# Kernel optimization log

Hardware: AMD Instinct MI355X
Metric: run time of the kernel (lower is better)

Reference implementation:

```python
import jax, jax.numpy as jnp
import numpy as np

H, W, C = 512, 512, 64
N_BOXES = 512
OUT_W = 32


def setup_inputs() -> dict:
    key = jax.random.key(0)
    k1, k2 = jax.random.split(key)
    feature_map = jax.random.normal(k1, (H, W, C), dtype=jnp.float32)
    # boxes are [cx, cy, w, h] as fractions of the image; uniform(0,1) is valid
    boxes = jax.random.uniform(k2, (N_BOXES, 4), dtype=jnp.float32)
    return {"feature_map": feature_map, "boxes": boxes, "output_width": OUT_W}


def reference(feature_map, boxes, output_width):
    """RoIAlign over a batch of boxes (vectorized version of roi_align_batch_serial)."""
    in_h, in_w, c = feature_map.shape
    out_h = out_w = output_width

    def roi_align_single(box):
        cx, cy, w, h = jnp.split(box, 4, axis=-1)
        x0 = cx - w / 2
        y0 = cy - h / 2
        w = jnp.maximum(w, 1e-6)
        h = jnp.maximum(h, 1e-6)
        x_scale = out_w / (w * in_w)
        y_scale = out_h / (h * in_h)
        return jax.image.scale_and_translate(
            feature_map,
            shape=(out_h, out_w, c),
            spatial_dims=(0, 1),
            scale=jnp.concatenate((y_scale, x_scale)),
            translation=jnp.concatenate((-y0 * out_h / h, -x0 * out_w / w)),
            method="linear",
            precision=jax.lax.Precision("fastest"),
        )

    # Same math as jax.lax.map(roi_align_single, boxes), but batched across boxes.
    return jax.vmap(roi_align_single)(boxes)  # [N, out_h, out_w, C]
```

## Files before the change

### kernel.cpp

```cpp
#include <hip/hip_runtime.h>


#define H_IN 512
#define W_IN 512
#define CH   64
#define NB   512
#define OW   32
#define WSTRIDE 33
#define WXS     40
#define TAPS_MAX 33
#define COLS_H  156
#define COLS_CL 146

__global__ __launch_bounds__(256) void roi_weights(const float* __restrict__ boxes,
                                                   float* __restrict__ wTab,
                                                   int* __restrict__ meta) {
    int tid = blockIdx.x * blockDim.x + threadIdx.x;
    if (tid >= NB * 2 * 32) return;
    int o   = tid & 31;
    int dim = (tid >> 5) & 1;
    int b   = tid >> 6;

    float cx = boxes[b * 4 + 0];
    float cy = boxes[b * 4 + 1];
    float bw = boxes[b * 4 + 2];
    float bh = boxes[b * 4 + 3];
    float cc = dim ? cx : cy;
    float sz = dim ? bw : bh;
    float lo = cc - sz * 0.5f;
    sz = fmaxf(sz, 1e-6f);

    float scale = (float)OW / (sz * (float)W_IN);
    float inv   = 1.0f / scale;
    float trans = (-lo * (float)OW) / sz;
    float s     = ((float)o + 0.5f) * inv - trans * inv - 0.5f;
    float ks    = fmaxf(inv, 1.0f);

    int i_lo = max((int)ceilf(s - ks), 0);
    int i_hi = min((int)floorf(s + ks), W_IN - 1);
    int cnt  = i_hi - i_lo + 1;
    if (cnt < 0) cnt = 0;
    if (cnt > TAPS_MAX) cnt = TAPS_MAX;

    float sum = 0.0f;
    for (int k = 0; k < cnt; ++k) {
        float x = fabsf(s - (float)(i_lo + k)) / ks;
        sum += fmaxf(0.0f, 1.0f - x);
    }
    bool ok = (sum > 1.1920929e-4f) && (s >= -0.5f) && (s <= (float)W_IN - 0.5f);

    float* wout = wTab + ((size_t)(dim * NB + b) * 32 + o) * WSTRIDE;
    for (int k = 0; k < TAPS_MAX; ++k) {
        float w = 0.0f;
        if (ok && k < cnt) {
            float x = fabsf(s - (float)(i_lo + k)) / ks;
            w = fmaxf(0.0f, 1.0f - x) / sum;
        }
        wout[k] = w;
    }
    int* m = meta + ((size_t)(dim * NB + b) * 32 + o) * 2;
    m[0] = i_lo;
    m[1] = ok ? cnt : 0;
}

__device__ __forceinline__ void gload16(const float* src, float* ldsDst) {
    __builtin_amdgcn_global_load_lds((const __attribute__((address_space(1))) void*)src,
                                     (__attribute__((address_space(3))) void*)ldsDst, 16, 0, 0);
}

__global__ __launch_bounds__(64) void roi_wave(const float* __restrict__ fm,
                                               const float* __restrict__ wTab,
                                               const int* __restrict__ meta,
                                               float* __restrict__ out) {
    __shared__ float sBuf[2][COLS_H * 16];
    __shared__ float sWx[8 * WXS];
    __shared__ float sWy[16 * WSTRIDE];
    __shared__ int   sMx[16];
    __shared__ int   sMyLC[16];
    __shared__ int   sU[4];

    int bid = blockIdx.x;
    int box = ((bid >> 8) << 3) | (bid & 7);
    int sub = (bid >> 3) & 31;
    int ox0 = (sub & 3) * 8;
    int ch0 = ((sub >> 2) & 3) * 16;
    int oy0 = (sub >> 4) * 16;
    int t   = threadIdx.x;

    const float* wxsrc = wTab + ((size_t)(NB + box) * 32 + ox0) * WSTRIDE;
    for (int i = t; i < 8 * WXS; i += 64) {
        int o = i / WXS, k = i - o * WXS;
        sWx[i] = (k < WSTRIDE) ? wxsrc[o * WSTRIDE + k] : 0.0f;
    }
    const float* wysrc = wTab + ((size_t)box * 32 + oy0) * WSTRIDE;
    for (int i = t; i < 16 * WSTRIDE; i += 64) sWy[i] = wysrc[i];
    if (t < 16) sMx[t] = meta[((size_t)(NB + box) * 32 + ox0) * 2 + t];
    if (t >= 16 && t < 32) {
        int k  = t - 16;
        int lo = meta[((size_t)box * 32 + oy0 + k) * 2];
        int cn = meta[((size_t)box * 32 + oy0 + k) * 2 + 1];
        sMyLC[k] = (lo & 0xffff) | (cn << 16);
    }
    __syncthreads();
    if (t == 0) {
        int lo = 0x7fffffff, hi = -1;
        for (int k = 0; k < 16; ++k) {
            int lc = sMyLC[k], c = lc >> 16;
            if (c > 0) { int l = lc & 0xffff; lo = min(lo, l); hi = max(hi, l + c); }
        }
        sU[0] = (hi > lo) ? lo : 0;
        sU[1] = (hi > lo) ? (hi - lo) : 0;
        int xlo = 0x7fffffff, xhi = -1;
        for (int k = 0; k < 8; ++k) {
            int c = sMx[2 * k + 1];
            if (c > 0) { int l = sMx[2 * k]; xlo = min(xlo, l); xhi = max(xhi, l + c); }
        }
        sU[2] = (xhi > xlo) ? xlo : 0;
        int cux = (xhi > xlo) ? (xhi - xlo) : 0;
        sU[3] = (cux > COLS_CL) ? COLS_CL : cux;
    }
    __syncthreads();
    int u0 = sU[0], cu = sU[1], xu0 = sU[2], cux = sU[3];

    int ox = t >> 3, cp = t & 7;
    int ix0rel = max(sMx[2 * ox] - xu0, 0);
    int cntx   = sMx[2 * ox + 1];
    int nch    = (cntx + 7) >> 3;

    int myLC[16];
    #pragma unroll
    for (int k = 0; k < 16; ++k) myLC[k] = sMyLC[k];

    float accA[16], accB[16];
    #pragma unroll
    for (int k = 0; k < 16; ++k) { accA[k] = 0.f; accB[k] = 0.f; }

    for (int i = t; i < 2 * 8 * 16; i += 64) {
        int b = i >> 7, col = (i >> 4) & 7, ch = i & 15;
        sBuf[b][(cux + col) * 16 + ch] = 0.0f;
    }

    const float* laneSrc = fm + (size_t)(xu0 + (t >> 2)) * CH + ch0 + (t & 3) * 4;
    int laneCol = t >> 2;

    if (cu > 0) {
        const float* rowSrc = laneSrc + (size_t)u0 * (W_IN * CH);
        for (int c0w = 0; c0w < cux; c0w += 16) {
            if (c0w + laneCol < cux) gload16(rowSrc + c0w * CH, &sBuf[0][c0w * 16]);
        }
    }
    __syncthreads();

    int cur = 0;
    for (int r = 0; r < cu; ++r) {
        if (r + 1 < cu) {
            const float* rowSrc = laneSrc + (size_t)(u0 + r + 1) * (W_IN * CH);
            float* dst = &sBuf[cur ^ 1][0];
            for (int c0w = 0; c0w < cux; c0w += 16) {
                if (c0w + laneCol < cux) gload16(rowSrc + c0w * CH, dst + c0w * 16);
            }
        }

        const float* wxp = &sWx[ox * WXS];
        const float* bp  = &sBuf[cur][0] + ix0rel * 16 + cp * 2;
        float xa = 0.f, xb = 0.f;
        for (int c = 0; c < nch; ++c) {
            float2 v[8];
            #pragma unroll
            for (int k = 0; k < 8; ++k) v[k] = *(const float2*)(bp + k * 16);
            float4 w0 = *(const float4*)(wxp + c * 8);
            float4 w1 = *(const float4*)(wxp + c * 8 + 4);
            xa = fmaf(w0.x, v[0].x, xa); xb = fmaf(w0.x, v[0].y, xb);
            xa = fmaf(w0.y, v[1].x, xa); xb = fmaf(w0.y, v[1].y, xb);
            xa = fmaf(w0.z, v[2].x, xa); xb = fmaf(w0.z, v[2].y, xb);
            xa = fmaf(w0.w, v[3].x, xa); xb = fmaf(w0.w, v[3].y, xb);
            xa = fmaf(w1.x, v[4].x, xa); xb = fmaf(w1.x, v[4].y, xb);
            xa = fmaf(w1.y, v[5].x, xa); xb = fmaf(w1.y, v[5].y, xb);
            xa = fmaf(w1.z, v[6].x, xa); xb = fmaf(w1.z, v[6].y, xb);
            xa = fmaf(w1.w, v[7].x, xa); xb = fmaf(w1.w, v[7].y, xb);
            bp += 128;
        }

        int iy = u0 + r;
        #pragma unroll
        for (int oy = 0; oy < 16; ++oy) {
            int lc = myLC[oy];
            int rr = iy - (lc & 0xffff);
            if ((unsigned)rr < (unsigned)(lc >> 16)) {
                float w = sWy[oy * WSTRIDE + rr];
                accA[oy] = fmaf(w, xa, accA[oy]);
                accB[oy] = fmaf(w, xb, accB[oy]);
            }
        }

        asm volatile("s_waitcnt vmcnt(0)" ::: "memory");
        cur ^= 1;
    }

    #pragma unroll
    for (int oy = 0; oy < 16; ++oy) {
        float* op = out + (((size_t)box * 32 + oy0 + oy) * 32 + ox0 + ox) * CH + ch0 + cp * 2;
        *(float2*)op = make_float2(accA[oy], accB[oy]);
    }
}

extern "C" void kernel_launch(void* const* d_in, const int* in_sizes, int n_in,
                              void* d_out, int out_size, void* d_ws, size_t ws_size,
                              hipStream_t stream) {
    const float* fm    = (const float*)d_in[0];
    const float* boxes = (const float*)d_in[1];

    float* wTab = (float*)d_ws;
    int*   meta = (int*)((char*)d_ws + (size_t)2 * NB * 32 * WSTRIDE * sizeof(float));

    roi_weights<<<(NB * 2 * 32 + 255) / 256, 256, 0, stream>>>(boxes, wTab, meta);
    roi_wave<<<NB * 32, 64, 0, stream>>>(fm, wTab, meta, (float*)d_out);
}
```

Measured before the change: 1.627 ms.

## Triple-buffer row staging with partial vmcnt waits and register-held x weights

Replaces the double-buffered row loop with a three-buffer pipeline that keeps two rows in flight. It waits with a vmcnt count equal to the per-row load count, selected by templating on the number of 16-column loads. The x-direction weights move from LDS into registers, read directly from a table whose row stride is padded to 40, and the x tap loop is fully unrolled with a guard. This is meant to hide global-to-LDS latency and cut LDS weight traffic, at the cost of more LDS per block, more registers, and a larger code size from the template switch.

```diff
diff --git a/kernel.cpp b/kernel.cpp
--- a/kernel.cpp
+++ b/kernel.cpp
@@ -6,10 +6,10 @@
 #define CH   64
 #define NB   512
 #define OW   32
-#define WSTRIDE 33
-#define WXS     40
+#define WG   40
+#define WYS  33
 #define TAPS_MAX 33
-#define COLS_H  156
+#define COLS_B 152
 #define COLS_CL 146
 
 __global__ __launch_bounds__(256) void roi_weights(const float* __restrict__ boxes,
@@ -49,8 +49,8 @@
     }
     bool ok = (sum > 1.1920929e-4f) && (s >= -0.5f) && (s <= (float)W_IN - 0.5f);
 
-    float* wout = wTab + ((size_t)(dim * NB + b) * 32 + o) * WSTRIDE;
-    for (int k = 0; k < TAPS_MAX; ++k) {
+    float* wout = wTab + ((size_t)(dim * NB + b) * 32 + o) * WG;
+    for (int k = 0; k < WG; ++k) {
         float w = 0.0f;
         if (ok && k < cnt) {
             float x = fabsf(s - (float)(i_lo + k)) / ks;
@@ -68,13 +68,38 @@
                                      (__attribute__((address_space(3))) void*)ldsDst, 16, 0, 0);
 }
 
-__global__ __launch_bounds__(64) void roi_wave(const float* __restrict__ fm,
-                                               const float* __restrict__ wTab,
-                                               const int* __restrict__ meta,
-                                               float* __restrict__ out) {
-    __shared__ float sBuf[2][COLS_H * 16];
-    __shared__ float sWx[8 * WXS];
-    __shared__ float sWy[16 * WSTRIDE];
+template<int N> __device__ __forceinline__ void wait_vm() {
+    if constexpr (N == 0)  asm volatile("s_waitcnt vmcnt(0)"  ::: "memory");
+    if constexpr (N == 1)  asm volatile("s_waitcnt vmcnt(1)"  ::: "memory");
+    if constexpr (N == 2)  asm volatile("s_waitcnt vmcnt(2)"  ::: "memory");
+    if constexpr (N == 3)  asm volatile("s_waitcnt vmcnt(3)"  ::: "memory");
+    if constexpr (N == 4)  asm volatile("s_waitcnt vmcnt(4)"  ::: "memory");
+    if constexpr (N == 5)  asm volatile("s_waitcnt vmcnt(5)"  ::: "memory");
+    if constexpr (N == 6)  asm volatile("s_waitcnt vmcnt(6)"  ::: "memory");
+    if constexpr (N == 7)  asm volatile("s_waitcnt vmcnt(7)"  ::: "memory");
+    if constexpr (N == 8)  asm volatile("s_waitcnt vmcnt(8)"  ::: "memory");
+    if constexpr (N == 9)  asm volatile("s_waitcnt vmcnt(9)"  ::: "memory");
+    if constexpr (N == 10) asm volatile("s_waitcnt vmcnt(10)" ::: "memory");
+}
+
+template<int NGL>
+__device__ __forceinline__ void stage_row(const float* rowSrc, float* dst,
+                                          int laneCol, int cux) {
+    #pragma unroll
+    for (int b = 0; b < NGL; ++b) {
+        if (b * 16 + laneCol < cux)
+            gload16(rowSrc + b * 16 * CH, dst + b * 256);
+    }
+}
+
+template<int N> struct IC { static constexpr int value = N; };
+
+__global__ __launch_bounds__(64, 2) void roi_pipe(const float* __restrict__ fm,
+                                                  const float* __restrict__ wTab,
+                                                  const int* __restrict__ meta,
+                                                  float* __restrict__ out) {
+    __shared__ float sBuf[3][COLS_B * 16];
+    __shared__ float sWy[16 * WYS];
     __shared__ int   sMx[16];
     __shared__ int   sMyLC[16];
     __shared__ int   sU[4];
@@ -87,13 +112,11 @@
     int oy0 = (sub >> 4) * 16;
     int t   = threadIdx.x;
 
-    const float* wxsrc = wTab + ((size_t)(NB + box) * 32 + ox0) * WSTRIDE;
-    for (int i = t; i < 8 * WXS; i += 64) {
-        int o = i / WXS, k = i - o * WXS;
-        sWx[i] = (k < WSTRIDE) ? wxsrc[o * WSTRIDE + k] : 0.0f;
-    }
-    const float* wysrc = wTab + ((size_t)box * 32 + oy0) * WSTRIDE;
-    for (int i = t; i < 16 * WSTRIDE; i += 64) sWy[i] = wysrc[i];
+    const float* wysrc = wTab + ((size_t)box * 32 + oy0) * WG;
+    for (int i = t; i < 16 * WYS; i += 64) {
+        int o = i / WYS, k = i - o * WYS;
+        sWy[i] = wysrc[o * WG + k];
+    }
     if (t < 16) sMx[t] = meta[((size_t)(NB + box) * 32 + ox0) * 2 + t];
     if (t >= 16 && t < 32) {
         int k  = t - 16;
@@ -127,6 +150,14 @@
     int cntx   = sMx[2 * ox + 1];
     int nch    = (cntx + 7) >> 3;
 
+    const float* wxg = wTab + ((size_t)(NB + box) * 32 + ox0 + ox) * WG;
+    float4 wr[10];
+    #pragma unroll
+    for (int c = 0; c < 5; ++c) {
+        wr[2 * c]     = *(const float4*)(wxg + c * 8);
+        wr[2 * c + 1] = *(const float4*)(wxg + c * 8 + 4);
+    }
+
     int myLC[16];
     #pragma unroll
     for (int k = 0; k < 16; ++k) myLC[k] = sMyLC[k];
@@ -135,66 +166,79 @@
     #pragma unroll
     for (int k = 0; k < 16; ++k) { accA[k] = 0.f; accB[k] = 0.f; }
 
-    for (int i = t; i < 2 * 8 * 16; i += 64) {
-        int b = i >> 7, col = (i >> 4) & 7, ch = i & 15;
-        sBuf[b][(cux + col) * 16 + ch] = 0.0f;
-    }
-
-    const float* laneSrc = fm + (size_t)(xu0 + (t >> 2)) * CH + ch0 + (t & 3) * 4;
+    for (int i = t; i < 3 * 8 * 16; i += 64) {
+        int b = i >> 7, rem = i & 127;
+        int cc = cux + (rem >> 4);
+        if (cc < COLS_B) sBuf[b][cc * 16 + (rem & 15)] = 0.0f;
+    }
+
     int laneCol = t >> 2;
-
-    if (cu > 0) {
-        const float* rowSrc = laneSrc + (size_t)u0 * (W_IN * CH);
-        for (int c0w = 0; c0w < cux; c0w += 16) {
-            if (c0w + laneCol < cux) gload16(rowSrc + c0w * CH, &sBuf[0][c0w * 16]);
-        }
-    }
+    const float* laneSrc = fm + (size_t)(xu0 + laneCol) * CH + ch0 + (t & 3) * 4;
     __syncthreads();
 
-    int cur = 0;
-    for (int r = 0; r < cu; ++r) {
-        if (r + 1 < cu) {
-            const float* rowSrc = laneSrc + (size_t)(u0 + r + 1) * (W_IN * CH);
-            float* dst = &sBuf[cur ^ 1][0];
-            for (int c0w = 0; c0w < cux; c0w += 16) {
-                if (c0w + laneCol < cux) gload16(rowSrc + c0w * CH, dst + c0w * 16);
+    int ngl = (cux + 15) >> 4;
+    if (cu > 0 && ngl > 0) {
+        auto run = [&](auto nglc) {
+            constexpr int NGL = decltype(nglc)::value;
+            stage_row<NGL>(laneSrc + (size_t)u0 * (W_IN * CH), sBuf[0], laneCol, cux);
+            if (cu > 1)
+                stage_row<NGL>(laneSrc + (size_t)(u0 + 1) * (W_IN * CH), sBuf[1], laneCol, cux);
+            float* bA = sBuf[0];
+            float* bB = sBuf[1];
+            float* bC = sBuf[2];
+            for (int r = 0; r < cu; ++r) {
+                wait_vm<NGL>();
+                if (r + 2 < cu)
+                    stage_row<NGL>(laneSrc + (size_t)(u0 + r + 2) * (W_IN * CH), bC, laneCol, cux);
+                __builtin_amdgcn_sched_barrier(0);
+
+                const float* bp = bA + ix0rel * 16 + cp * 2;
+                float xa = 0.f, xb = 0.f;
+                #pragma unroll
+                for (int c = 0; c < 5; ++c) {
+                    if (c < nch) {
+                        float2 v[8];
+                        #pragma unroll
+                        for (int k = 0; k < 8; ++k) v[k] = *(const float2*)(bp + (c * 8 + k) * 16);
+                        float4 w0 = wr[2 * c], w1 = wr[2 * c + 1];
+                        xa = fmaf(w0.x, v[0].x, xa); xb = fmaf(w0.x, v[0].y, xb);
+                        xa = fmaf(w0.y, v[1].x, xa); xb = fmaf(w0.y, v[1].y, xb);
+                        xa = fmaf(w0.z, v[2].x, xa); xb = fmaf(w0.z, v[2].y, xb);
+                        xa = fmaf(w0.w, v[3].x, xa); xb = fmaf(w0.w, v[3].y, xb);
+                        xa = fmaf(w1.x, v[4].x, xa); xb = fmaf(w1.x, v[4].y, xb);
+                        xa = fmaf(w1.y, v[5].x, xa); xb = fmaf(w1.y, v[5].y, xb);
+                        xa = fmaf(w1.z, v[6].x, xa); xb = fmaf(w1.z, v[6].y, xb);
+                        xa = fmaf(w1.w, v[7].x, xa); xb = fmaf(w1.w, v[7].y, xb);
+                    }
+                }
+
+                int iy = u0 + r;
+                #pragma unroll
+                for (int oy = 0; oy < 16; ++oy) {
+                    int lc = myLC[oy];
+                    int rr = iy - (lc & 0xffff);
+                    if ((unsigned)rr < (unsigned)(lc >> 16)) {
+                        float w = sWy[oy * WYS + rr];
+                        accA[oy] = fmaf(w, xa, accA[oy]);
+                        accB[oy] = fmaf(w, xb, accB[oy]);
+                    }
+                }
+
+                float* tmp = bA; bA = bB; bB = bC; bC = tmp;
             }
-        }
-
-        const float* wxp = &sWx[ox * WXS];
-        const float* bp  = &sBuf[cur][0] + ix0rel * 16 + cp * 2;
-        float xa = 0.f, xb = 0.f;
-        for (int c = 0; c < nch; ++c) {
-            float2 v[8];
-            #pragma unroll
-            for (int k = 0; k < 8; ++k) v[k] = *(const float2*)(bp + k * 16);
-            float4 w0 = *(const float4*)(wxp + c * 8);
-            float4 w1 = *(const float4*)(wxp + c * 8 + 4);
-            xa = fmaf(w0.x, v[0].x, xa); xb = fmaf(w0.x, v[0].y, xb);
-            xa = fmaf(w0.y, v[1].x, xa); xb = fmaf(w0.y, v[1].y, xb);
-            xa = fmaf(w0.z, v[2].x, xa); xb = fmaf(w0.z, v[2].y, xb);
-            xa = fmaf(w0.w, v[3].x, xa); xb = fmaf(w0.w, v[3].y, xb);
-            xa = fmaf(w1.x, v[4].x, xa); xb = fmaf(w1.x, v[4].y, xb);
-            xa = fmaf(w1.y, v[5].x, xa); xb = fmaf(w1.y, v[5].y, xb);
-            xa = fmaf(w1.z, v[6].x, xa); xb = fmaf(w1.z, v[6].y, xb);
-            xa = fmaf(w1.w, v[7].x, xa); xb = fmaf(w1.w, v[7].y, xb);
-            bp += 128;
-        }
-
-        int iy = u0 + r;
-        #pragma unroll
-        for (int oy = 0; oy < 16; ++oy) {
-            int lc = myLC[oy];
-            int rr = iy - (lc & 0xffff);
-            if ((unsigned)rr < (unsigned)(lc >> 16)) {
-                float w = sWy[oy * WSTRIDE + rr];
-                accA[oy] = fmaf(w, xa, accA[oy]);
-                accB[oy] = fmaf(w, xb, accB[oy]);
-            }
-        }
-
-        asm volatile("s_waitcnt vmcnt(0)" ::: "memory");
-        cur ^= 1;
+        };
+        switch (ngl) {
+            case 1:  run(IC<1>{});  break;
+            case 2:  run(IC<2>{});  break;
+            case 3:  run(IC<3>{});  break;
+            case 4:  run(IC<4>{});  break;
+            case 5:  run(IC<5>{});  break;
+            case 6:  run(IC<6>{});  break;
+            case 7:  run(IC<7>{});  break;
+            case 8:  run(IC<8>{});  break;
+            case 9:  run(IC<9>{});  break;
+            default: run(IC<10>{}); break;
+        }
     }
 
     #pragma unroll
@@ -211,8 +255,8 @@
     const float* boxes = (const float*)d_in[1];
 
     float* wTab = (float*)d_ws;
-    int*   meta = (int*)((char*)d_ws + (size_t)2 * NB * 32 * WSTRIDE * sizeof(float));
+    int*   meta = (int*)((char*)d_ws + (size_t)2 * NB * 32 * WG * sizeof(float));
 
     roi_weights<<<(NB * 2 * 32 + 255) / 256, 256, 0, stream>>>(boxes, wTab, meta);
-    roi_wave<<<NB * 32, 64, 0, stream>>>(fm, wTab, meta, (float*)d_out);
-}
+    roi_pipe<<<NB * 32, 64, 0, stream>>>(fm, wTab, meta, (float*)d_out);
+}
```

Result: slower. 1.917 ms (+17.8%).
